# Kernel optimization log

Measured on AMD Instinct MI355X. Metric: run time of the kernel, lower is better.

The kernel has to match this reference:

```python
import jax, jax.numpy as jnp
import numpy as np

N = 250000
CIN, COUT = 16, 32
D, H, W = 32, 360, 360
EPS = 1e-3
SLOPE = 0.01


def _build_nbr(z, y, x, lut, offsets):
    total = D * H * W
    maps = []
    for dz, dy, dx in offsets:
        nz, ny, nx = z + dz, y + dy, x + dx
        inb = (nz >= 0) & (nz < D) & (ny >= 0) & (ny < H) & (nx >= 0) & (nx < W)
        nlin = np.clip(nz * (H * W) + ny * W + nx, 0, total - 1)
        idx = np.where(inb, lut[nlin], -1).astype(np.int32)
        maps.append(idx)
    return np.stack(maps, axis=0)  # [9, N]


def setup_inputs() -> dict:
    key = jax.random.key(0)
    ks = jax.random.split(key, 6)
    rng = np.random.default_rng(0)
    total = D * H * W
    lin = rng.choice(total, size=N, replace=False)
    z = lin // (H * W)
    rem = lin % (H * W)
    y = rem // W
    x = rem % W
    lut = np.full(total, -1, dtype=np.int32)
    lut[lin] = np.arange(N, dtype=np.int32)
    # kernel (1,3,3): offsets over (h, w); kernel (3,1,3): offsets over (d, w)
    off133 = [(0, dy, dx) for dy in (-1, 0, 1) for dx in (-1, 0, 1)]
    off313 = [(dz, 0, dx) for dz in (-1, 0, 1) for dx in (-1, 0, 1)]
    nbr133 = jnp.asarray(_build_nbr(z, y, x, lut, off133))
    nbr313 = jnp.asarray(_build_nbr(z, y, x, lut, off313))
    features = jax.random.normal(ks[0], (N, CIN), dtype=jnp.float32)
    w = lambda k, ci, co: jax.random.normal(k, (9, ci, co), dtype=jnp.float32) * 0.05
    return {
        "features": features,
        "nbr133": nbr133,
        "nbr313": nbr313,
        "conv1_w": w(ks[1], CIN, COUT),
        "conv12_w": w(ks[2], COUT, COUT),
        "conv2_w": w(ks[3], CIN, COUT),
        "conv3_w": w(ks[4], COUT, COUT),
        "bn0_g": jnp.ones((COUT,), jnp.float32), "bn0_b": jnp.zeros((COUT,), jnp.float32),
        "bn02_g": jnp.ones((COUT,), jnp.float32), "bn02_b": jnp.zeros((COUT,), jnp.float32),
        "bn1_g": jnp.ones((COUT,), jnp.float32), "bn1_b": jnp.zeros((COUT,), jnp.float32),
        "bn2_g": jnp.ones((COUT,), jnp.float32), "bn2_b": jnp.zeros((COUT,), jnp.float32),
    }


def _subm_conv(feats, nbr, w):
    # feats [N,Cin], nbr [K,N] int32 (-1 = no neighbor), w [K,Cin,Cout]
    valid = (nbr >= 0)[..., None]
    g = jnp.where(valid, feats[jnp.clip(nbr, 0)], 0.0)  # [K,N,Cin] gather
    return jnp.einsum("knc,kcd->nd", g, w)  # GEMM + scatter-accumulate


def _bn(xf, g, b):
    # BatchNorm1d training-mode: biased batch stats over N
    m = jnp.mean(xf, axis=0)
    v = jnp.mean(jnp.square(xf - m), axis=0)
    return (xf - m) * jax.lax.rsqrt(v + EPS) * g + b


def _lrelu(xf):
    return jnp.where(xf >= 0, xf, SLOPE * xf)


def reference(features, nbr133, nbr313, conv1_w, conv12_w, conv2_w, conv3_w,
              bn0_g, bn0_b, bn02_g, bn02_b, bn1_g, bn1_b, bn2_g, bn2_b):
    # shortcut branch: conv1x3 -> act -> bn -> conv3x1 -> act -> bn
    sc = _subm_conv(features, nbr133, conv1_w)
    sc = _bn(_lrelu(sc), bn0_g, bn0_b)
    sc = _subm_conv(sc, nbr313, conv12_w)
    sc = _bn(_lrelu(sc), bn02_g, bn02_b)
    # main branch: conv3x1 -> act -> bn -> conv1x3 -> act -> bn
    res = _subm_conv(features, nbr313, conv2_w)
    res = _bn(_lrelu(res), bn1_g, bn1_b)
    res = _subm_conv(res, nbr133, conv3_w)
    res = _bn(_lrelu(res), bn2_g, bn2_b)
    return res + sc
```

## Files before the change

kernel.cpp:

```cpp
#include <hip/hip_runtime.h>

#define EPS 1e-3f
#define SLOPE 0.01f
#define TPW 4
#define NBANK 16

typedef __attribute__((ext_vector_type(8))) short s8v;
typedef __attribute__((ext_vector_type(4))) float f4v;

union U4S8 {
  uint4 u;
  s8v s;
};

static __device__ inline unsigned f2bf(float x) {
  unsigned u = __float_as_uint(x);
  return (u + 0x7fffu + ((u >> 16) & 1u)) >> 16;
}
static __device__ inline float bf_lo(unsigned u) {
  return __uint_as_float(u << 16);
}
static __device__ inline float bf_hi(unsigned u) {
  return __uint_as_float(u & 0xffff0000u);
}

__global__ __launch_bounds__(256) void prep_kernel(
    const float* __restrict__ features, uint4* __restrict__ fbf, int n8,
    const float* __restrict__ w1, const float* __restrict__ w2,
    uint4* __restrict__ tab, float* __restrict__ sums, uint4* __restrict__ r0,
    uint4* __restrict__ r1, uint4* __restrict__ r2, int nc) {
  const int b = blockIdx.x;
  const int tid = threadIdx.x;
  if (b < nc) {
    int i = b * 256 + tid;
    if (i < n8) {
      const float4* p = (const float4*)features + (size_t)i * 2;
      float4 a = p[0], bb = p[1];
      uint4 o;
      o.x = f2bf(a.x) | (f2bf(a.y) << 16);
      o.y = f2bf(a.z) | (f2bf(a.w) << 16);
      o.z = f2bf(bb.x) | (f2bf(bb.y) << 16);
      o.w = f2bf(bb.z) | (f2bf(bb.w) << 16);
      fbf[i] = o;
    }
  } else if (b == nc) {
#pragma unroll
    for (int i = 0; i < 16; i++) sums[i * 256 + tid] = 0.f;
    uint4 z = {0u, 0u, 0u, 0u};
    if (tid < 2) r0[tid] = z;
    else if (tid < 6) r1[tid - 2] = z;
    else if (tid < 10) r2[tid - 6] = z;
  } else if (tid < 64) {
    const int sb = b - nc - 1;
    const int conv = sb / 10, slot = sb % 10;
    const float* w = conv ? w2 : w1;
    const int T = slot >> 1, f = slot & 1;
    const int g = tid >> 4, c = tid & 15;
    s8v t;
#pragma unroll
    for (int j = 0; j < 8; j++) {
      int kl = g * 8 + j;
      int tap = 2 * T + (kl >> 4);
      int ci = kl & 15;
      t[j] = (short)(tap < 9 ? f2bf(w[(tap * 16 + ci) * 32 + 2 * c + f]) : 0);
    }
    U4S8 u;
    u.s = t;
    tab[(conv * 10 + slot) * 64 + tid] = u.u;
  }
}

__global__ __launch_bounds__(64) void build_tab_k2(
    const float* __restrict__ w12, const float* __restrict__ w3,
    const float* __restrict__ sums1, const float* __restrict__ sums2,
    const float* __restrict__ g0, const float* __restrict__ b0,
    const float* __restrict__ g1, const float* __restrict__ b1,
    uint4* __restrict__ tab, int n) {
  __shared__ float stl[64];
  const int conv = blockIdx.x / 20, slot = blockIdx.x % 20;
  const float* w = conv ? w3 : w12;
  const float* sums = conv ? sums2 : sums1;
  const float* bn_g = conv ? g1 : g0;
  const float* bn_b = conv ? b1 : b0;
  const int lane = threadIdx.x;
  if (lane < 32) {
    float ssum = 0.f, qsum = 0.f;
#pragma unroll
    for (int bk = 0; bk < NBANK; bk++) {
      ssum += sums[bk * 64 + lane];
      qsum += sums[bk * 64 + 32 + lane];
    }
    float inv_n = 1.0f / (float)n;
    float m = ssum * inv_n;
    float v = qsum * inv_n - m * m;
    float s = bn_g[lane] * rsqrtf(v + EPS);
    stl[lane] = s;
    stl[32 + lane] = bn_b[lane] - m * s;
  }
  __syncthreads();
  const int g = lane >> 4, c = lane & 15;
  s8v t;
  if (slot < 18) {
    const int k = slot >> 1, f = slot & 1;
#pragma unroll
    for (int j = 0; j < 8; j++) {
      int ci = g * 8 + j;
      t[j] = (short)f2bf(w[(k * 32 + ci) * 32 + 2 * c + f] * stl[ci]);
    }
  } else {
    const int f = slot - 18;
#pragma unroll
    for (int j = 0; j < 8; j++) {
      int kk = g * 8 + j;
      if (kk < 9) {
        float a = 0.f;
        for (int ci = 0; ci < 32; ci++)
          a += stl[32 + ci] * w[(kk * 32 + ci) * 32 + 2 * c + f];
        t[j] = (short)f2bf(a);
      } else {
        t[j] = 0;
      }
    }
  }
  U4S8 u;
  u.s = t;
  tab[(conv * 20 + slot) * 64 + lane] = u.u;
}

template <bool PAIRED>
__global__ __launch_bounds__(256, 3) void conv_mfma(
    const unsigned short* __restrict__ src0, const int* __restrict__ nbr0,
    const uint4* __restrict__ tab0, unsigned short* __restrict__ dst0,
    float* __restrict__ osums0, const unsigned short* __restrict__ src1,
    const int* __restrict__ nbr1, const uint4* __restrict__ tab1,
    unsigned short* __restrict__ dst1, float* __restrict__ osums1, int n,
    int gb) {
  constexpr int NS = PAIRED ? 5 : 9;
  constexpr int NSLOT = PAIRED ? 10 : 20;
  __shared__ uint4 bwl[NSLOT * 64];
  __shared__ float redl[4 * 64];

  const int tid = threadIdx.x;
  const bool second = (int)blockIdx.x >= gb;
  const unsigned short* src = second ? src1 : src0;
  const int* nbr = second ? nbr1 : nbr0;
  const uint4* tab = second ? tab1 : tab0;
  unsigned short* dst = second ? dst1 : dst0;
  float* osums = second ? osums1 : osums0;

  for (int i = tid; i < NSLOT * 64; i += 256) bwl[i] = tab[i];
  __syncthreads();

  const int lane = tid & 63;
  const int wv = tid >> 6;
  const int g = lane >> 4;
  const int c = lane & 15;

  s8v bbias0, bbias1;
  if (!PAIRED) {
    U4S8 x;
    x.u = bwl[18 * 64 + lane];
    bbias0 = x.s;
    x.u = bwl[19 * 64 + lane];
    bbias1 = x.s;
  }

  const int bid = second ? (int)blockIdx.x - gb : (int)blockIdx.x;
  const int wbase = bid * (64 * TPW) + wv * (16 * TPW);

  float s0 = 0.f, s1 = 0.f, q0 = 0.f, q1 = 0.f;

  int jj[9], jjn[9];
  {
    int pt = wbase + c;
    bool a = pt < n;
#pragma unroll
    for (int k = 0; k < 9; k++) jj[k] = a ? nbr[(size_t)k * n + pt] : -1;
  }

#pragma unroll 1
  for (int t = 0; t < TPW; t++) {
    const int pbase = wbase + t * 16;
    {
      int pt = pbase + 16 + c;
      bool a = (t + 1 < TPW) && (pt < n);
#pragma unroll
      for (int k = 0; k < 9; k++) jjn[k] = a ? nbr[(size_t)k * n + pt] : -1;
    }
    unsigned vmask = 0;
    if (!PAIRED) {
#pragma unroll
      for (int k = 0; k < 9; k++) vmask |= (jj[k] >= 0 ? 1u : 0u) << k;
    }

    bool slot_on[NS];
#pragma unroll
    for (int s = 0; s < NS; s++) {
      if (PAIRED) {
        int jA = jj[2 * s];
        int jB = jj[(2 * s + 1 < 9) ? 2 * s + 1 : 8];
        slot_on[s] = __ballot(jA >= 0 || jB >= 0) != 0ull;
      } else {
        slot_on[s] = __ballot(jj[s] >= 0) != 0ull;
      }
    }

    uint4 ga[NS];
#pragma unroll
    for (int s = 0; s < NS; s++) {
      if (slot_on[s]) {
        int jr;
        if (PAIRED) {
          int jA = jj[2 * s];
          int jB = jj[(2 * s + 1 < 9) ? 2 * s + 1 : 8];
          jr = (g & 2) ? jB : jA;
        } else {
          jr = jj[s];
        }
        unsigned jc = jr < 0 ? (unsigned)n : (unsigned)jr;
        const uint4* p =
            (const uint4*)src +
            (PAIRED ? ((size_t)jc * 2 + (g & 1)) : ((size_t)jc * 4 + g));
        ga[s] = p[0];
      }
    }
    __builtin_amdgcn_sched_barrier(0);

    f4v acc0 = {0.f, 0.f, 0.f, 0.f};
    f4v acc1 = {0.f, 0.f, 0.f, 0.f};
#pragma unroll
    for (int s = 0; s < NS; s++) {
      if (slot_on[s]) {
        U4S8 a;
        a.u = ga[s];
        U4S8 b0, b1;
        b0.u = bwl[(s * 2 + 0) * 64 + lane];
        b1.u = bwl[(s * 2 + 1) * 64 + lane];
        acc0 = __builtin_amdgcn_mfma_f32_16x16x32_bf16(a.s, b0.s, acc0, 0, 0, 0);
        acc1 = __builtin_amdgcn_mfma_f32_16x16x32_bf16(a.s, b1.s, acc1, 0, 0, 0);
      }
    }
    if (!PAIRED) {
      s8v av;
#pragma unroll
      for (int j = 0; j < 8; j++) {
        unsigned kk = (unsigned)(g * 8 + j);
        unsigned bit = (kk < 32u) ? ((vmask >> kk) & 1u) : 0u;
        av[j] = (short)(bit ? 0x3F80 : 0);
      }
      acc0 = __builtin_amdgcn_mfma_f32_16x16x32_bf16(av, bbias0, acc0, 0, 0, 0);
      acc1 = __builtin_amdgcn_mfma_f32_16x16x32_bf16(av, bbias1, acc1, 0, 0, 0);
    }

#pragma unroll
    for (int r = 0; r < 4; r++) {
      float x = acc0[r];
      x = fmaxf(x, SLOPE * x);
      acc0[r] = x;
      s0 += x;
      q0 = fmaf(x, x, q0);
      float y = acc1[r];
      y = fmaxf(y, SLOPE * y);
      acc1[r] = y;
      s1 += y;
      q1 = fmaf(y, y, q1);
    }

#pragma unroll
    for (int r = 0; r < 4; r++) {
      int p = pbase + g * 4 + r;
      if (p < n)
        ((unsigned*)dst)[(size_t)p * 16 + c] =
            f2bf(acc0[r]) | (f2bf(acc1[r]) << 16);
    }
#pragma unroll
    for (int k = 0; k < 9; k++) jj[k] = jjn[k];
  }

  s0 += __shfl_xor(s0, 16, 64);
  s0 += __shfl_xor(s0, 32, 64);
  s1 += __shfl_xor(s1, 16, 64);
  s1 += __shfl_xor(s1, 32, 64);
  q0 += __shfl_xor(q0, 16, 64);
  q0 += __shfl_xor(q0, 32, 64);
  q1 += __shfl_xor(q1, 16, 64);
  q1 += __shfl_xor(q1, 32, 64);
  if (lane < 16) {
    redl[wv * 64 + 2 * c] = s0;
    redl[wv * 64 + 2 * c + 1] = s1;
    redl[wv * 64 + 32 + 2 * c] = q0;
    redl[wv * 64 + 32 + 2 * c + 1] = q1;
  }
  __syncthreads();
  if (tid < 64) {
    float t = redl[tid] + redl[64 + tid] + redl[128 + tid] + redl[192 + tid];
    atomicAdd(&osums[(bid & (NBANK - 1)) * 64 + tid], t);
  }
}

__global__ __launch_bounds__(256) void final_kernel(
    const uint4* __restrict__ z12, const uint4* __restrict__ z3,
    float* __restrict__ out, const float* __restrict__ sumsA,
    const float* __restrict__ gA, const float* __restrict__ bA,
    const float* __restrict__ sumsB, const float* __restrict__ gB,
    const float* __restrict__ bB, int n) {
  __shared__ float st[128];
  const int tid = threadIdx.x;
  if (tid < 32) {
    float sa = 0.f, qa = 0.f, sb = 0.f, qb = 0.f;
#pragma unroll
    for (int bk = 0; bk < NBANK; bk++) {
      sa += sumsA[bk * 64 + tid];
      qa += sumsA[bk * 64 + 32 + tid];
      sb += sumsB[bk * 64 + tid];
      qb += sumsB[bk * 64 + 32 + tid];
    }
    float inv_n = 1.0f / (float)n;
    float m = sa * inv_n;
    float v = qa * inv_n - m * m;
    float s = gA[tid] * rsqrtf(v + EPS);
    st[tid] = s;
    st[32 + tid] = bA[tid] - m * s;
    m = sb * inv_n;
    v = qb * inv_n - m * m;
    s = gB[tid] * rsqrtf(v + EPS);
    st[64 + tid] = s;
    st[96 + tid] = bB[tid] - m * s;
  }
  __syncthreads();
  const int total = n * 4;
  for (int i = blockIdx.x * 256 + tid; i < total; i += gridDim.x * 256) {
    int c0 = (i & 3) * 8;
    uint4 a = z12[i], b = z3[i];
    float4 r0, r1;
    r0.x = bf_lo(a.x) * st[c0 + 0] + st[32 + c0 + 0] + bf_lo(b.x) * st[64 + c0 + 0] + st[96 + c0 + 0];
    r0.y = bf_hi(a.x) * st[c0 + 1] + st[32 + c0 + 1] + bf_hi(b.x) * st[64 + c0 + 1] + st[96 + c0 + 1];
    r0.z = bf_lo(a.y) * st[c0 + 2] + st[32 + c0 + 2] + bf_lo(b.y) * st[64 + c0 + 2] + st[96 + c0 + 2];
    r0.w = bf_hi(a.y) * st[c0 + 3] + st[32 + c0 + 3] + bf_hi(b.y) * st[64 + c0 + 3] + st[96 + c0 + 3];
    r1.x = bf_lo(a.z) * st[c0 + 4] + st[32 + c0 + 4] + bf_lo(b.z) * st[64 + c0 + 4] + st[96 + c0 + 4];
    r1.y = bf_hi(a.z) * st[c0 + 5] + st[32 + c0 + 5] + bf_hi(b.z) * st[64 + c0 + 5] + st[96 + c0 + 5];
    r1.z = bf_lo(a.w) * st[c0 + 6] + st[32 + c0 + 6] + bf_lo(b.w) * st[64 + c0 + 6] + st[96 + c0 + 6];
    r1.w = bf_hi(a.w) * st[c0 + 7] + st[32 + c0 + 7] + bf_hi(b.w) * st[64 + c0 + 7] + st[96 + c0 + 7];
    ((float4*)out)[2 * i + 0] = r0;
    ((float4*)out)[2 * i + 1] = r1;
  }
}

extern "C" void kernel_launch(void* const* d_in, const int* in_sizes, int n_in,
                              void* d_out, int out_size, void* d_ws,
                              size_t ws_size, hipStream_t stream) {
  const float* features = (const float*)d_in[0];
  const int* nbr133 = (const int*)d_in[1];
  const int* nbr313 = (const int*)d_in[2];
  const float* conv1_w = (const float*)d_in[3];
  const float* conv12_w = (const float*)d_in[4];
  const float* conv2_w = (const float*)d_in[5];
  const float* conv3_w = (const float*)d_in[6];
  const float* bn0_g = (const float*)d_in[7];
  const float* bn0_b = (const float*)d_in[8];
  const float* bn02_g = (const float*)d_in[9];
  const float* bn02_b = (const float*)d_in[10];
  const float* bn1_g = (const float*)d_in[11];
  const float* bn1_b = (const float*)d_in[12];
  const float* bn2_g = (const float*)d_in[13];
  const float* bn2_b = (const float*)d_in[14];
  float* out = (float*)d_out;

  const int n = in_sizes[0] / 16;
  char* ws = (char*)d_ws;
  const size_t A = (size_t)n * 64 + 64;

  unsigned short* fbf = (unsigned short*)ws;
  unsigned short* z12 = (unsigned short*)ws;
  unsigned short* zA1 = (unsigned short*)(ws + A);
  unsigned short* zA2 = (unsigned short*)(ws + 2 * A);
  unsigned short* z3 = (unsigned short*)(ws + 3 * A);
  float* sums = (float*)(ws + 4 * A);
  uint4* tabK1 = (uint4*)(ws + 4 * A + 4 * NBANK * 64 * 4);
  uint4* tabK2 = tabK1 + 20 * 64;

  const int n8 = n * 2;
  const int nc = (n8 + 255) / 256;
  prep_kernel<<<nc + 21, 256, 0, stream>>>(
      features, (uint4*)fbf, n8, conv1_w, conv2_w, tabK1, sums,
      (uint4*)(ws + (size_t)n * 32),
      (uint4*)(ws + A + (size_t)n * 64),
      (uint4*)(ws + 2 * A + (size_t)n * 64),
      nc);

  const int gb = (n + 64 * TPW - 1) / (64 * TPW);
  conv_mfma<true><<<2 * gb, 256, 0, stream>>>(
      fbf, nbr133, tabK1, zA1, sums + 0, fbf, nbr313, tabK1 + 10 * 64, zA2,
      sums + 1024, n, gb);
  build_tab_k2<<<40, 64, 0, stream>>>(conv12_w, conv3_w, sums + 0, sums + 1024,
                                      bn0_g, bn0_b, bn1_g, bn1_b, tabK2, n);
  conv_mfma<false><<<2 * gb, 256, 0, stream>>>(
      zA1, nbr313, tabK2, z12, sums + 2048, zA2, nbr133, tabK2 + 20 * 64, z3,
      sums + 3072, n, gb);
  final_kernel<<<1024, 256, 0, stream>>>((const uint4*)z12, (const uint4*)z3,
                                         out, sums + 2048, bn02_g, bn02_b,
                                         sums + 3072, bn2_g, bn2_b, n);
}
```

Before: 73.85 us.

## Fuse second conv pass with final BN via grid-wide barrier and register-held outputs

Merges the second convolution pass and the final BN+add kernel into one persistent kernel. Each block processes both convolutions for its points, holds the bf16 activations in registers, accumulates BN stats, then waits on a global atomic counter barrier before applying the normalization and writing output directly. This removes a kernel launch and the round-trip of z12/z3 through global memory. It depends on all blocks being co-resident (about 489 blocks at 2 per CU), so it risks deadlock, and the higher register use may lower occupancy.

```diff
diff --git a/kernel.cpp b/kernel.cpp
--- a/kernel.cpp
+++ b/kernel.cpp
@@ -3,6 +3,7 @@
 #define EPS 1e-3f
 #define SLOPE 0.01f
 #define TPW 4
+#define TPWF 8
 #define NBANK 16
 
 typedef __attribute__((ext_vector_type(8))) short s8v;
@@ -28,7 +29,8 @@
     const float* __restrict__ features, uint4* __restrict__ fbf, int n8,
     const float* __restrict__ w1, const float* __restrict__ w2,
     uint4* __restrict__ tab, float* __restrict__ sums, uint4* __restrict__ r0,
-    uint4* __restrict__ r1, uint4* __restrict__ r2, int nc) {
+    uint4* __restrict__ r1, uint4* __restrict__ r2, unsigned* __restrict__ ctr,
+    int nc) {
   const int b = blockIdx.x;
   const int tid = threadIdx.x;
   if (b < nc) {
@@ -50,6 +52,7 @@
     if (tid < 2) r0[tid] = z;
     else if (tid < 6) r1[tid - 2] = z;
     else if (tid < 10) r2[tid - 6] = z;
+    else if (tid == 10) *ctr = 0u;
   } else if (tid < 64) {
     const int sb = b - nc - 1;
     const int conv = sb / 10, slot = sb % 10;
@@ -298,22 +301,174 @@
   }
 }
 
-__global__ __launch_bounds__(256) void final_kernel(
-    const uint4* __restrict__ z12, const uint4* __restrict__ z3,
-    float* __restrict__ out, const float* __restrict__ sumsA,
-    const float* __restrict__ gA, const float* __restrict__ bA,
-    const float* __restrict__ sumsB, const float* __restrict__ gB,
-    const float* __restrict__ bB, int n) {
+__global__ __launch_bounds__(256, 2) void conv_mfma_final(
+    const unsigned short* __restrict__ srcA, const int* __restrict__ nbrA,
+    const unsigned short* __restrict__ srcB, const int* __restrict__ nbrB,
+    const uint4* __restrict__ tab, float* __restrict__ sumsA,
+    float* __restrict__ sumsB, const float* __restrict__ gA,
+    const float* __restrict__ bA, const float* __restrict__ gB,
+    const float* __restrict__ bB, float* __restrict__ out,
+    unsigned* __restrict__ ctr, int n) {
+  __shared__ uint4 bwl[40 * 64];
+  __shared__ float redl[4 * 64];
   __shared__ float st[128];
+
   const int tid = threadIdx.x;
+  for (int i = tid; i < 40 * 64; i += 256) bwl[i] = tab[i];
+  __syncthreads();
+
+  const int lane = tid & 63;
+  const int wv = tid >> 6;
+  const int g = lane >> 4;
+  const int c = lane & 15;
+  const int bid = (int)blockIdx.x;
+  const int wbase = bid * (64 * TPWF) + wv * (16 * TPWF);
+
+  unsigned zheld[2][TPWF][4];
+
+#pragma unroll
+  for (int conv = 0; conv < 2; conv++) {
+    const unsigned short* src = conv ? srcB : srcA;
+    const int* nbr = conv ? nbrB : nbrA;
+    float* osums = conv ? sumsB : sumsA;
+    const int toff = conv * 20 * 64;
+
+    s8v bbias0, bbias1;
+    {
+      U4S8 x;
+      x.u = bwl[toff + 18 * 64 + lane];
+      bbias0 = x.s;
+      x.u = bwl[toff + 19 * 64 + lane];
+      bbias1 = x.s;
+    }
+
+    float s0 = 0.f, s1 = 0.f, q0 = 0.f, q1 = 0.f;
+    int jj[9], jjn[9];
+    {
+      int pt = wbase + c;
+      bool a = pt < n;
+#pragma unroll
+      for (int k = 0; k < 9; k++) jj[k] = a ? nbr[(size_t)k * n + pt] : -1;
+    }
+
+#pragma unroll
+    for (int t = 0; t < TPWF; t++) {
+      const int pbase = wbase + t * 16;
+      {
+        int pt = pbase + 16 + c;
+        bool a = (t + 1 < TPWF) && (pt < n);
+#pragma unroll
+        for (int k = 0; k < 9; k++)
+          jjn[k] = a ? nbr[(size_t)k * n + pt] : -1;
+      }
+      unsigned vmask = 0;
+#pragma unroll
+      for (int k = 0; k < 9; k++) vmask |= (jj[k] >= 0 ? 1u : 0u) << k;
+
+      bool slot_on[9];
+#pragma unroll
+      for (int s = 0; s < 9; s++) slot_on[s] = __ballot(jj[s] >= 0) != 0ull;
+
+      uint4 ga[9];
+#pragma unroll
+      for (int s = 0; s < 9; s++) {
+        if (slot_on[s]) {
+          int jr = jj[s];
+          unsigned jc = jr < 0 ? (unsigned)n : (unsigned)jr;
+          ga[s] = ((const uint4*)src)[(size_t)jc * 4 + g];
+        }
+      }
+      __builtin_amdgcn_sched_barrier(0);
+
+      f4v acc0 = {0.f, 0.f, 0.f, 0.f};
+      f4v acc1 = {0.f, 0.f, 0.f, 0.f};
+#pragma unroll
+      for (int s = 0; s < 9; s++) {
+        if (slot_on[s]) {
+          U4S8 a;
+          a.u = ga[s];
+          U4S8 b0, b1;
+          b0.u = bwl[toff + (s * 2 + 0) * 64 + lane];
+          b1.u = bwl[toff + (s * 2 + 1) * 64 + lane];
+          acc0 =
+              __builtin_amdgcn_mfma_f32_16x16x32_bf16(a.s, b0.s, acc0, 0, 0, 0);
+          acc1 =
+              __builtin_amdgcn_mfma_f32_16x16x32_bf16(a.s, b1.s, acc1, 0, 0, 0);
+        }
+      }
+      {
+        s8v av;
+#pragma unroll
+        for (int j = 0; j < 8; j++) {
+          unsigned kk = (unsigned)(g * 8 + j);
+          unsigned bit = (kk < 32u) ? ((vmask >> kk) & 1u) : 0u;
+          av[j] = (short)(bit ? 0x3F80 : 0);
+        }
+        acc0 =
+            __builtin_amdgcn_mfma_f32_16x16x32_bf16(av, bbias0, acc0, 0, 0, 0);
+        acc1 =
+            __builtin_amdgcn_mfma_f32_16x16x32_bf16(av, bbias1, acc1, 0, 0, 0);
+      }
+
+#pragma unroll
+      for (int r = 0; r < 4; r++) {
+        float x = acc0[r];
+        x = fmaxf(x, SLOPE * x);
+        s0 += x;
+        q0 = fmaf(x, x, q0);
+        float y = acc1[r];
+        y = fmaxf(y, SLOPE * y);
+        s1 += y;
+        q1 = fmaf(y, y, q1);
+        zheld[conv][t][r] = f2bf(x) | (f2bf(y) << 16);
+      }
+#pragma unroll
+      for (int k = 0; k < 9; k++) jj[k] = jjn[k];
+    }
+
+    s0 += __shfl_xor(s0, 16, 64);
+    s0 += __shfl_xor(s0, 32, 64);
+    s1 += __shfl_xor(s1, 16, 64);
+    s1 += __shfl_xor(s1, 32, 64);
+    q0 += __shfl_xor(q0, 16, 64);
+    q0 += __shfl_xor(q0, 32, 64);
+    q1 += __shfl_xor(q1, 16, 64);
+    q1 += __shfl_xor(q1, 32, 64);
+    __syncthreads();
+    if (lane < 16) {
+      redl[wv * 64 + 2 * c] = s0;
+      redl[wv * 64 + 2 * c + 1] = s1;
+      redl[wv * 64 + 32 + 2 * c] = q0;
+      redl[wv * 64 + 32 + 2 * c + 1] = q1;
+    }
+    __syncthreads();
+    if (tid < 64) {
+      float t = redl[tid] + redl[64 + tid] + redl[128 + tid] + redl[192 + tid];
+      atomicAdd(&osums[(bid & (NBANK - 1)) * 64 + tid], t);
+    }
+  }
+
+  __syncthreads();
+  if (tid == 0) {
+    __hip_atomic_fetch_add(ctr, 1u, __ATOMIC_ACQ_REL, __HIP_MEMORY_SCOPE_AGENT);
+    while (__hip_atomic_load(ctr, __ATOMIC_ACQUIRE, __HIP_MEMORY_SCOPE_AGENT) <
+           gridDim.x)
+      __builtin_amdgcn_s_sleep(2);
+  }
+  __syncthreads();
+
   if (tid < 32) {
     float sa = 0.f, qa = 0.f, sb = 0.f, qb = 0.f;
 #pragma unroll
     for (int bk = 0; bk < NBANK; bk++) {
-      sa += sumsA[bk * 64 + tid];
-      qa += sumsA[bk * 64 + 32 + tid];
-      sb += sumsB[bk * 64 + tid];
-      qb += sumsB[bk * 64 + 32 + tid];
+      sa += __hip_atomic_load(&sumsA[bk * 64 + tid], __ATOMIC_RELAXED,
+                              __HIP_MEMORY_SCOPE_AGENT);
+      qa += __hip_atomic_load(&sumsA[bk * 64 + 32 + tid], __ATOMIC_RELAXED,
+                              __HIP_MEMORY_SCOPE_AGENT);
+      sb += __hip_atomic_load(&sumsB[bk * 64 + tid], __ATOMIC_RELAXED,
+                              __HIP_MEMORY_SCOPE_AGENT);
+      qb += __hip_atomic_load(&sumsB[bk * 64 + 32 + tid], __ATOMIC_RELAXED,
+                              __HIP_MEMORY_SCOPE_AGENT);
     }
     float inv_n = 1.0f / (float)n;
     float m = sa * inv_n;
@@ -328,21 +483,26 @@
     st[96 + tid] = bB[tid] - m * s;
   }
   __syncthreads();
-  const int total = n * 4;
-  for (int i = blockIdx.x * 256 + tid; i < total; i += gridDim.x * 256) {
-    int c0 = (i & 3) * 8;
-    uint4 a = z12[i], b = z3[i];
-    float4 r0, r1;
-    r0.x = bf_lo(a.x) * st[c0 + 0] + st[32 + c0 + 0] + bf_lo(b.x) * st[64 + c0 + 0] + st[96 + c0 + 0];
-    r0.y = bf_hi(a.x) * st[c0 + 1] + st[32 + c0 + 1] + bf_hi(b.x) * st[64 + c0 + 1] + st[96 + c0 + 1];
-    r0.z = bf_lo(a.y) * st[c0 + 2] + st[32 + c0 + 2] + bf_lo(b.y) * st[64 + c0 + 2] + st[96 + c0 + 2];
-    r0.w = bf_hi(a.y) * st[c0 + 3] + st[32 + c0 + 3] + bf_hi(b.y) * st[64 + c0 + 3] + st[96 + c0 + 3];
-    r1.x = bf_lo(a.z) * st[c0 + 4] + st[32 + c0 + 4] + bf_lo(b.z) * st[64 + c0 + 4] + st[96 + c0 + 4];
-    r1.y = bf_hi(a.z) * st[c0 + 5] + st[32 + c0 + 5] + bf_hi(b.z) * st[64 + c0 + 5] + st[96 + c0 + 5];
-    r1.z = bf_lo(a.w) * st[c0 + 6] + st[32 + c0 + 6] + bf_lo(b.w) * st[64 + c0 + 6] + st[96 + c0 + 6];
-    r1.w = bf_hi(a.w) * st[c0 + 7] + st[32 + c0 + 7] + bf_hi(b.w) * st[64 + c0 + 7] + st[96 + c0 + 7];
-    ((float4*)out)[2 * i + 0] = r0;
-    ((float4*)out)[2 * i + 1] = r1;
+
+  const int c2 = 2 * c;
+  const float sA0 = st[c2], tA0 = st[32 + c2];
+  const float sB0 = st[64 + c2], tB0 = st[96 + c2];
+  const float sA1 = st[c2 + 1], tA1 = st[32 + c2 + 1];
+  const float sB1 = st[64 + c2 + 1], tB1 = st[96 + c2 + 1];
+#pragma unroll
+  for (int t = 0; t < TPWF; t++) {
+    const int pbase = wbase + t * 16;
+#pragma unroll
+    for (int r = 0; r < 4; r++) {
+      int p = pbase + g * 4 + r;
+      if (p < n) {
+        unsigned za = zheld[0][t][r], zb = zheld[1][t][r];
+        float2 o;
+        o.x = bf_lo(za) * sA0 + tA0 + bf_lo(zb) * sB0 + tB0;
+        o.y = bf_hi(za) * sA1 + tA1 + bf_hi(zb) * sB1 + tB1;
+        ((float2*)out)[(size_t)p * 16 + c] = o;
+      }
+    }
   }
 }
 
@@ -371,13 +531,12 @@
   const size_t A = (size_t)n * 64 + 64;
 
   unsigned short* fbf = (unsigned short*)ws;
-  unsigned short* z12 = (unsigned short*)ws;
   unsigned short* zA1 = (unsigned short*)(ws + A);
   unsigned short* zA2 = (unsigned short*)(ws + 2 * A);
-  unsigned short* z3 = (unsigned short*)(ws + 3 * A);
   float* sums = (float*)(ws + 4 * A);
   uint4* tabK1 = (uint4*)(ws + 4 * A + 4 * NBANK * 64 * 4);
   uint4* tabK2 = tabK1 + 20 * 64;
+  unsigned* ctr = (unsigned*)(tabK2 + 40 * 64);
 
   const int n8 = n * 2;
   const int nc = (n8 + 255) / 256;
@@ -386,7 +545,7 @@
       (uint4*)(ws + (size_t)n * 32),
       (uint4*)(ws + A + (size_t)n * 64),
       (uint4*)(ws + 2 * A + (size_t)n * 64),
-      nc);
+      ctr, nc);
 
   const int gb = (n + 64 * TPW - 1) / (64 * TPW);
   conv_mfma<true><<<2 * gb, 256, 0, stream>>>(
@@ -394,10 +553,8 @@
       sums + 1024, n, gb);
   build_tab_k2<<<40, 64, 0, stream>>>(conv12_w, conv3_w, sums + 0, sums + 1024,
                                       bn0_g, bn0_b, bn1_g, bn1_b, tabK2, n);
-  conv_mfma<false><<<2 * gb, 256, 0, stream>>>(
-      zA1, nbr313, tabK2, z12, sums + 2048, zA2, nbr133, tabK2 + 20 * 64, z3,
-      sums + 3072, n, gb);
-  final_kernel<<<1024, 256, 0, stream>>>((const uint4*)z12, (const uint4*)z3,
-                                         out, sums + 2048, bn02_g, bn02_b,
-                                         sums + 3072, bn2_g, bn2_b, n);
-}
+  const int gb2 = (n + 64 * TPWF - 1) / (64 * TPWF);
+  conv_mfma_final<<<gb2, 256, 0, stream>>>(
+      zA1, nbr313, zA2, nbr133, tabK2, sums + 2048, sums + 3072, bn02_g,
+      bn02_b, bn2_g, bn2_b, out, ctr, n);
+}
```

New measurement: 134.9 us. 82.6% more time.

## Software-pipeline neighbor gathers one tile ahead in sparse conv MFMA kernel

Applied to the files above, without the earlier changes.

Restructures the per-wave tile loop into a double-buffered software pipeline. Neighbor indices are loaded two tiles ahead and feature gathers are issued one tile ahead, so gather latency overlaps the MFMA work of the current tile. The loop is now fully unrolled. The paired conv kernel also gets a higher minimum-blocks launch bound of 4. The costs are higher register pressure from holding two gather buffers, and possible spills or lower occupancy.

```diff
diff --git a/kernel.cpp b/kernel.cpp
--- a/kernel.cpp
+++ b/kernel.cpp
@@ -127,8 +127,54 @@
   tab[(conv * 20 + slot) * 64 + lane] = u.u;
 }
 
-template <bool PAIRED>
-__global__ __launch_bounds__(256, 3) void conv_mfma(
+__device__ __forceinline__ void load_idx(const int* __restrict__ nbr, int n,
+                                         int pt, int (&JJ)[9]) {
+  bool a = pt < n;
+#pragma unroll
+  for (int k = 0; k < 9; k++) JJ[k] = a ? nbr[(size_t)k * n + pt] : -1;
+}
+
+template <bool PAIRED, int NS>
+__device__ __forceinline__ void produce(const unsigned short* __restrict__ src,
+                                        int n, int g, const int (&JJ)[9],
+                                        uint4 (&GA)[NS], unsigned& VM,
+                                        unsigned& SON) {
+  VM = 0;
+#pragma unroll
+  for (int k = 0; k < 9; k++) VM |= (JJ[k] >= 0 ? 1u : 0u) << k;
+  SON = 0;
+#pragma unroll
+  for (int s = 0; s < NS; s++) {
+    bool on;
+    if (PAIRED) {
+      int jA = JJ[2 * s];
+      int jB = JJ[(2 * s + 1 < 9) ? 2 * s + 1 : 8];
+      on = __ballot(jA >= 0 || jB >= 0) != 0ull;
+    } else {
+      on = __ballot(JJ[s] >= 0) != 0ull;
+    }
+    SON |= (on ? 1u : 0u) << s;
+  }
+#pragma unroll
+  for (int s = 0; s < NS; s++) {
+    if (SON & (1u << s)) {
+      int jr;
+      if (PAIRED) {
+        int jA = JJ[2 * s];
+        int jB = JJ[(2 * s + 1 < 9) ? 2 * s + 1 : 8];
+        jr = (g & 2) ? jB : jA;
+      } else {
+        jr = JJ[s];
+      }
+      unsigned jc = jr < 0 ? (unsigned)n : (unsigned)jr;
+      GA[s] = ((const uint4*)src)[PAIRED ? ((size_t)jc * 2 + (g & 1))
+                                         : ((size_t)jc * 4 + g)];
+    }
+  }
+}
+
+template <bool PAIRED, int MINB>
+__global__ __launch_bounds__(256, MINB) void conv_mfma(
     const unsigned short* __restrict__ src0, const int* __restrict__ nbr0,
     const uint4* __restrict__ tab0, unsigned short* __restrict__ dst0,
     float* __restrict__ osums0, const unsigned short* __restrict__ src1,
@@ -170,69 +216,32 @@
 
   float s0 = 0.f, s1 = 0.f, q0 = 0.f, q1 = 0.f;
 
-  int jj[9], jjn[9];
-  {
-    int pt = wbase + c;
-    bool a = pt < n;
-#pragma unroll
-    for (int k = 0; k < 9; k++) jj[k] = a ? nbr[(size_t)k * n + pt] : -1;
-  }
-
-#pragma unroll 1
+  int jjb[2][9];
+  uint4 gab[2][NS];
+  unsigned vmb[2], sonb[2];
+
+  load_idx(nbr, n, wbase + c, jjb[0]);
+  load_idx(nbr, n, wbase + 16 + c, jjb[1]);
+  produce<PAIRED, NS>(src, n, g, jjb[0], gab[0], vmb[0], sonb[0]);
+
+#pragma unroll
   for (int t = 0; t < TPW; t++) {
+    const int cur = t & 1, nxt = 1 - (t & 1);
     const int pbase = wbase + t * 16;
-    {
-      int pt = pbase + 16 + c;
-      bool a = (t + 1 < TPW) && (pt < n);
-#pragma unroll
-      for (int k = 0; k < 9; k++) jjn[k] = a ? nbr[(size_t)k * n + pt] : -1;
-    }
-    unsigned vmask = 0;
-    if (!PAIRED) {
-#pragma unroll
-      for (int k = 0; k < 9; k++) vmask |= (jj[k] >= 0 ? 1u : 0u) << k;
-    }
-
-    bool slot_on[NS];
-#pragma unroll
-    for (int s = 0; s < NS; s++) {
-      if (PAIRED) {
-        int jA = jj[2 * s];
-        int jB = jj[(2 * s + 1 < 9) ? 2 * s + 1 : 8];
-        slot_on[s] = __ballot(jA >= 0 || jB >= 0) != 0ull;
-      } else {
-        slot_on[s] = __ballot(jj[s] >= 0) != 0ull;
-      }
-    }
-
-    uint4 ga[NS];
-#pragma unroll
-    for (int s = 0; s < NS; s++) {
-      if (slot_on[s]) {
-        int jr;
-        if (PAIRED) {
-          int jA = jj[2 * s];
-          int jB = jj[(2 * s + 1 < 9) ? 2 * s + 1 : 8];
-          jr = (g & 2) ? jB : jA;
-        } else {
-          jr = jj[s];
-        }
-        unsigned jc = jr < 0 ? (unsigned)n : (unsigned)jr;
-        const uint4* p =
-            (const uint4*)src +
-            (PAIRED ? ((size_t)jc * 2 + (g & 1)) : ((size_t)jc * 4 + g));
-        ga[s] = p[0];
-      }
-    }
+
+    if (t + 2 < TPW)
+      load_idx(nbr, n, pbase + 32 + c, jjb[cur]);
+    if (t + 1 < TPW)
+      produce<PAIRED, NS>(src, n, g, jjb[nxt], gab[nxt], vmb[nxt], sonb[nxt]);
     __builtin_amdgcn_sched_barrier(0);
 
     f4v acc0 = {0.f, 0.f, 0.f, 0.f};
     f4v acc1 = {0.f, 0.f, 0.f, 0.f};
 #pragma unroll
     for (int s = 0; s < NS; s++) {
-      if (slot_on[s]) {
+      if (sonb[cur] & (1u << s)) {
         U4S8 a;
-        a.u = ga[s];
+        a.u = gab[cur][s];
         U4S8 b0, b1;
         b0.u = bwl[(s * 2 + 0) * 64 + lane];
         b1.u = bwl[(s * 2 + 1) * 64 + lane];
@@ -241,6 +250,7 @@
       }
     }
     if (!PAIRED) {
+      unsigned vmask = vmb[cur];
       s8v av;
 #pragma unroll
       for (int j = 0; j < 8; j++) {
@@ -273,8 +283,6 @@
         ((unsigned*)dst)[(size_t)p * 16 + c] =
             f2bf(acc0[r]) | (f2bf(acc1[r]) << 16);
     }
-#pragma unroll
-    for (int k = 0; k < 9; k++) jj[k] = jjn[k];
   }
 
   s0 += __shfl_xor(s0, 16, 64);
@@ -389,12 +397,12 @@
       nc);
 
   const int gb = (n + 64 * TPW - 1) / (64 * TPW);
-  conv_mfma<true><<<2 * gb, 256, 0, stream>>>(
+  conv_mfma<true, 4><<<2 * gb, 256, 0, stream>>>(
       fbf, nbr133, tabK1, zA1, sums + 0, fbf, nbr313, tabK1 + 10 * 64, zA2,
       sums + 1024, n, gb);
   build_tab_k2<<<40, 64, 0, stream>>>(conv12_w, conv3_w, sums + 0, sums + 1024,
                                       bn0_g, bn0_b, bn1_g, bn1_b, tabK2, n);
-  conv_mfma<false><<<2 * gb, 256, 0, stream>>>(
+  conv_mfma<false, 3><<<2 * gb, 256, 0, stream>>>(
       zA1, nbr313, tabK2, z12, sums + 2048, zA2, nbr133, tabK2 + 20 * 64, z3,
       sums + 3072, n, gb);
   final_kernel<<<1024, 256, 0, stream>>>((const uint4*)z12, (const uint4*)z3,
```

New measurement: 76.87 us. +4.1%, slower.
